# Optimization experiments

Hardware: AMD Instinct MI355X
Metric: run time of the kernel (lower is better)

The kernel has to match this reference:

```python
import jax, jax.numpy as jnp
import numpy as np

B, S, D = 1, 2048, 2048      # batch, seq, hidden_dim
DF = 768                      # moe intermediate (per routed expert)
DSH = 2048                    # shared-expert intermediate
E, K = 32, 8                  # num routed experts, top_k
BLK = 128                     # fp8 block-scale size
CAP = 1024
T = B * S


def _dequant(w, s, blk=BLK):
    # w: [E, M, N] fp8 values (stored fp32), s: [E, M/blk, N/blk] block scales
    Eh, M, N = w.shape
    Mb, Nb = s.shape[1], s.shape[2]
    return (w.reshape(Eh, Mb, blk, Nb, blk) * s[:, :, None, :, None]).reshape(Eh, M, N)


def setup_inputs() -> dict:
    key = jax.random.key(0)
    ks = jax.random.split(key, 13)
    n = lambda k, shp, sc=0.02: jax.random.normal(k, shp, jnp.float32) * sc
    u = lambda k, shp: jax.random.uniform(k, shp, jnp.float32, 0.005, 0.02)
    return {
        "hidden_states": jax.random.normal(ks[0], (B, S, D), jnp.float32),
        "router_w": n(ks[1], (E, D)),
        # raw fp8-value weights (simulated as fp32 integers-in-range values) + block scale_inv
        "wg_fp8": jax.random.normal(ks[2], (E, DF, D), jnp.float32),
        "sg": u(ks[3], (E, DF // BLK, D // BLK)),
        "wu_fp8": jax.random.normal(ks[4], (E, DF, D), jnp.float32),
        "su": u(ks[5], (E, DF // BLK, D // BLK)),
        "wd_fp8": jax.random.normal(ks[6], (E, D, DF), jnp.float32),
        "sd": u(ks[7], (E, D // BLK, DF // BLK)),
        "ws_gate": n(ks[8], (DSH, D)),
        "ws_up": n(ks[9], (DSH, D)),
        "ws_down": n(ks[10], (D, DSH)),
        "w_shared_gate": n(ks[11], (1, D)),
    }


def reference(hidden_states, router_w, wg_fp8, sg, wu_fp8, su, wd_fp8, sd,
              ws_gate, ws_up, ws_down, w_shared_gate):
    x = hidden_states.reshape(-1, D)  # [T, D]

    # shared expert (SwiGLU) + its sigmoid gate
    shared = (jax.nn.silu(x @ ws_gate.T) * (x @ ws_up.T)) @ ws_down.T
    sh_gate = jax.nn.sigmoid(x @ w_shared_gate.T)  # [T, 1]

    # router: softmax -> top-k -> renormalize (Qwen MoE gate)
    probs = jax.nn.softmax(x @ router_w.T, axis=-1)          # [T, E]
    rw, sel = jax.lax.top_k(probs, K)                        # [T, K]
    rw = rw / jnp.sum(rw, axis=-1, keepdims=True)

    # capacity-based dispatch (replaces the python per-expert loop; same math)
    flat_e = sel.reshape(-1)                                 # [T*K]
    oh = jax.nn.one_hot(flat_e, E, dtype=jnp.int32)
    pos = jnp.sum(jnp.cumsum(oh, axis=0) * oh, axis=-1) - 1  # position within expert
    keep = (pos < CAP)
    pos_c = jnp.minimum(pos, CAP)                            # overflow -> scratch slot CAP
    tok = jnp.arange(T * K) // K                             # owning token of each (t,k) pair

    buf = jnp.zeros((E, CAP + 1, D), x.dtype).at[flat_e, pos_c].set(x[tok])

    # block-scale dequant (fp8*scale_inv), then per-expert SwiGLU
    Wg = _dequant(wg_fp8, sg)
    Wu = _dequant(wu_fp8, su)
    Wd = _dequant(wd_fp8, sd)
    g = jnp.einsum('ecd,efd->ecf', buf, Wg)
    up = jnp.einsum('ecd,efd->ecf', buf, Wu)
    h = jax.nn.silu(g) * up
    y = jnp.einsum('ecf,edf->ecd', h, Wd)                    # [E, CAP+1, D]

    # weighted scatter-add back to tokens (index_add_ equivalent)
    y_tok = y[flat_e, pos_c]                                 # [T*K, D]
    w_tok = rw.reshape(-1) * keep.astype(x.dtype)
    out = jax.ops.segment_sum(y_tok * w_tok[:, None], tok, num_segments=T)

    out = out + sh_gate * shared
    return out.reshape(B, S, D)
```

## Files before the change

### kernel.cpp

```cpp
#include <hip/hip_runtime.h>
#include <hip/hip_bf16.h>


#define TT   2048
#define DD   2048
#define DFF  768
#define DSH  2048
#define EE   32
#define KTOP 8
#define CAP  1024

typedef _Float16 half8  __attribute__((ext_vector_type(8)));
typedef _Float16 half4v __attribute__((ext_vector_type(4)));
typedef float    f32x4  __attribute__((ext_vector_type(4)));

__global__ __launch_bounds__(256) void k_init(int* __restrict__ cnt,
                                              int* __restrict__ slot_tok) {
  int i = blockIdx.x * 256 + threadIdx.x;
  if (i < EE * CAP) slot_tok[i] = 0;
  if (i < EE) cnt[i] = 0;
}

__global__ __launch_bounds__(256) void k_cast(const float* __restrict__ in,
                                              _Float16* __restrict__ out) {
  int i = blockIdx.x * 256 + threadIdx.x;
  float4 v = ((const float4*)in)[i];
  half4v h = { (_Float16)v.x, (_Float16)v.y, (_Float16)v.z, (_Float16)v.w };
  ((half4v*)out)[i] = h;
}

__global__ __launch_bounds__(64) void k_router(
    const float* __restrict__ x, const float* __restrict__ rw,
    const float* __restrict__ wshg,
    float* __restrict__ shg, int* __restrict__ cnt,
    int* __restrict__ slot_tok, float* __restrict__ slot_w,
    int* __restrict__ slot_pair, int* __restrict__ pair_pos) {
  int t = blockIdx.x;
  int lane = threadIdx.x;
  const float* xr = x + (size_t)t * DD;
  float xv[32];
#pragma unroll
  for (int j = 0; j < 32; ++j) xv[j] = xr[lane + j * 64];

  __shared__ float lg[EE];
  for (int e = 0; e < EE; ++e) {
    const float* we = rw + (size_t)e * DD;
    float s = 0.f;
#pragma unroll
    for (int j = 0; j < 32; ++j) s += xv[j] * we[lane + j * 64];
#pragma unroll
    for (int off = 32; off > 0; off >>= 1) s += __shfl_down(s, off);
    if (lane == 0) lg[e] = s;
  }
  {
    float s = 0.f;
#pragma unroll
    for (int j = 0; j < 32; ++j) s += xv[j] * wshg[lane + j * 64];
#pragma unroll
    for (int off = 32; off > 0; off >>= 1) s += __shfl_down(s, off);
    if (lane == 0) shg[t] = 1.f / (1.f + expf(-s));
  }
  if (lane == 0) {
    unsigned used = 0;
    int sel[KTOP];
    float val[KTOP];
    for (int k = 0; k < KTOP; ++k) {
      float bv = -1e30f; int bi = 0;
      for (int e = 0; e < EE; ++e)
        if (!((used >> e) & 1) && lg[e] > bv) { bv = lg[e]; bi = e; }
      used |= (1u << bi);
      sel[k] = bi; val[k] = bv;
    }
    float mx = val[0], sum = 0.f;
    for (int k = 0; k < KTOP; ++k) { val[k] = expf(val[k] - mx); sum += val[k]; }
    float inv = 1.f / sum;
    for (int k = 0; k < KTOP; ++k) {
      int e = sel[k];
      int pos = atomicAdd(&cnt[e], 1);
      pair_pos[t * KTOP + k] = pos;
      if (pos < CAP) {
        slot_tok[e * CAP + pos] = t;
        slot_w[e * CAP + pos] = val[k] * inv;
        slot_pair[e * CAP + pos] = t * KTOP + k;
      }
    }
  }
}

template<bool DUAL, bool GATHER, int EPI, int NPB, int MBB, int KDIM>
__global__ __launch_bounds__(256, 2) void k_gemm(
    const _Float16* __restrict__ A,
    const float* __restrict__ B0f, const float* __restrict__ B1f,
    const float* __restrict__ S0, const float* __restrict__ S1,
    int sCols, int sStrideE,
    _Float16* __restrict__ OutH,
    int ldA, int ldOut,
    long long strideAE, long long strideBE, long long strideOE,
    const int* __restrict__ cnt,
    const int* __restrict__ slot_tok, const float* __restrict__ slot_w) {
  constexpr int BK = 64;
  constexpr int KT = KDIM / BK;
  constexpr int NF = DUAL ? 2 : 4;
  constexpr int BN = DUAL ? 64 : 128;
  constexpr int BCH = DUAL ? 4 : 8;

  const int f = blockIdx.x;
  const int xcd = f & 7;
  const int t0 = f >> 3;
  const int mb = t0 % MBB;
  const int pp = t0 / MBB;
  const int p  = pp * 8 + xcd;
  const int nb = p % NPB;
  const int e  = p / NPB;

  int rows = cnt[e] > CAP ? CAP : cnt[e];
  const int rowBase = mb * 128;
  if (rowBase >= rows) return;
  const int nBase = nb * BN;

  const int tid = threadIdx.x;
  const int lane = tid & 63;
  const int wave = tid >> 6;
  const int wr = wave >> 1;
  const int wc = wave & 1;

  __shared__ __align__(16) _Float16 sA[3][8192];
  __shared__ __align__(16) _Float16 sB[2][8192];

  const _Float16* Ae = A + (GATHER ? 0 : (long long)e * strideAE);
  const float* B0e = B0f + (long long)e * strideBE;
  const float* B1e = DUAL ? (B1f + (long long)e * strideBE) : nullptr;
  const float* S0e = S0 + (long long)e * sStrideE;
  const float* S1e = DUAL ? (S1 + (long long)e * sStrideE) : nullptr;
  const int sRow = (nBase >> 7) * sCols;

  int aByte[4];
#pragma unroll
  for (int i = 0; i < 4; ++i) {
    int c = tid + i * 256;
    int row = c >> 3;
    int colB = ((c & 7) << 4) ^ ((row & 7) << 4);
    int src = GATHER ? slot_tok[e * CAP + rowBase + row] : (rowBase + row);
    aByte[i] = src * (2 * ldA) + colB;
  }
  int bOff[BCH], wByte[BCH];
#pragma unroll
  for (int i = 0; i < BCH; ++i) {
    int c = tid + i * 256;
    int rn = c >> 4;
    int c4 = (c & 15) << 2;
    bOff[i] = (nBase + rn) * KDIM + c4;
    wByte[i] = ((rn << 7) + (c4 << 1)) ^ ((rn & 7) << 4);
  }

  f32x4 accG[4][NF];
  f32x4 accU[DUAL ? 4 : 1][NF];
#pragma unroll
  for (int m = 0; m < 4; ++m)
#pragma unroll
    for (int n = 0; n < NF; ++n) {
      accG[m][n] = (f32x4){0.f, 0.f, 0.f, 0.f};
      if constexpr (DUAL) accU[m][n] = (f32x4){0.f, 0.f, 0.f, 0.f};
    }

  auto stageA = [&](int kt, int buf) {
#pragma unroll
    for (int i = 0; i < 4; ++i) {
      __builtin_amdgcn_global_load_lds(
          (const __attribute__((address_space(1))) void*)
              ((const char*)Ae + aByte[i] + kt * (BK * 2)),
          (__attribute__((address_space(3))) void*)&sA[buf][(tid + i * 256) * 8],
          16, 0, 0);
    }
  };
  auto loadB = [&](int kt, float4 (&r0)[BCH], float4 (&r1)[BCH]) {
    const int ko = kt * BK;
#pragma unroll
    for (int i = 0; i < BCH; ++i) r0[i] = *(const float4*)(B0e + bOff[i] + ko);
    if constexpr (DUAL) {
#pragma unroll
      for (int i = 0; i < BCH; ++i) r1[i] = *(const float4*)(B1e + bOff[i] + ko);
    }
  };
  auto storeB = [&](int kt, float4 (&r0)[BCH], float4 (&r1)[BCH]) {
    float s0 = S0e[sRow + (kt >> 1)];
    float s1 = DUAL ? S1e[sRow + (kt >> 1)] : 0.f;
    char* base = (char*)&sB[kt & 1][0];
#pragma unroll
    for (int i = 0; i < BCH; ++i) {
      half4v h = { (_Float16)(r0[i].x * s0), (_Float16)(r0[i].y * s0),
                   (_Float16)(r0[i].z * s0), (_Float16)(r0[i].w * s0) };
      *(half4v*)(base + wByte[i]) = h;
      if constexpr (DUAL) {
        half4v h1 = { (_Float16)(r1[i].x * s1), (_Float16)(r1[i].y * s1),
                      (_Float16)(r1[i].z * s1), (_Float16)(r1[i].w * s1) };
        *(half4v*)(base + 8192 + wByte[i]) = h1;
      }
    }
  };
  auto computeTile = [&](int ia, int ib) {
    const char* pA = (const char*)&sA[ia][0];
    const char* pB = (const char*)&sB[ib][0];
#pragma unroll
    for (int kk = 0; kk < 2; ++kk) {
      const int koff = kk * 32 + (lane >> 4) * 8;
      half8 a[4];
#pragma unroll
      for (int m = 0; m < 4; ++m) {
        int r = wr * 64 + m * 16 + (lane & 15);
        int byt = ((r << 7) + (koff << 1)) ^ ((r & 7) << 4);
        a[m] = *(const half8*)(pA + byt);
      }
      if constexpr (DUAL) {
        half8 bg[2], bu[2];
#pragma unroll
        for (int n = 0; n < 2; ++n) {
          int rn = wc * 32 + n * 16 + (lane & 15);
          int byt = ((rn << 7) + (koff << 1)) ^ ((rn & 7) << 4);
          bg[n] = *(const half8*)(pB + byt);
          bu[n] = *(const half8*)(pB + 8192 + byt);
        }
#pragma unroll
        for (int m = 0; m < 4; ++m)
#pragma unroll
          for (int n = 0; n < 2; ++n) {
            accG[m][n] = __builtin_amdgcn_mfma_f32_16x16x32_f16(a[m], bg[n], accG[m][n], 0, 0, 0);
            accU[m][n] = __builtin_amdgcn_mfma_f32_16x16x32_f16(a[m], bu[n], accU[m][n], 0, 0, 0);
          }
      } else {
        half8 b[4];
#pragma unroll
        for (int n = 0; n < 4; ++n) {
          int rn = wc * 64 + n * 16 + (lane & 15);
          int byt = ((rn << 7) + (koff << 1)) ^ ((rn & 7) << 4);
          b[n] = *(const half8*)(pB + byt);
        }
#pragma unroll
        for (int m = 0; m < 4; ++m)
#pragma unroll
          for (int n = 0; n < 4; ++n)
            accG[m][n] = __builtin_amdgcn_mfma_f32_16x16x32_f16(a[m], b[n], accG[m][n], 0, 0, 0);
      }
    }
  };

  float4 rbE0[BCH], rbE1[BCH], rbO0[BCH], rbO1[BCH];

  loadB(0, rbE0, rbE1);
  loadB(1, rbO0, rbO1);
  stageA(0, 0);
  stageA(1, 1);
  __builtin_amdgcn_sched_barrier(0);
  storeB(0, rbE0, rbE1);
  asm volatile("s_waitcnt lgkmcnt(0)" ::: "memory");
  asm volatile("s_waitcnt vmcnt(4)" ::: "memory");
  __builtin_amdgcn_s_barrier();
  __builtin_amdgcn_sched_barrier(0);

  int bufC = 0, bufW = 2;
  for (int kt = 0; kt < KT; ++kt) {
    if (kt + 2 < KT) {
      stageA(kt + 2, bufW);
      if (kt & 1) loadB(kt + 2, rbO0, rbO1);
      else        loadB(kt + 2, rbE0, rbE1);
      __builtin_amdgcn_sched_barrier(0);
    }
    computeTile(bufC, kt & 1);
    if (kt + 1 < KT) {
      if (kt & 1) storeB(kt + 1, rbE0, rbE1);
      else        storeB(kt + 1, rbO0, rbO1);
    }
    asm volatile("s_waitcnt lgkmcnt(0)" ::: "memory");
    if (kt + 2 < KT) { asm volatile("s_waitcnt vmcnt(12)" ::: "memory"); }
    else             { asm volatile("s_waitcnt vmcnt(0)"  ::: "memory"); }
    __builtin_amdgcn_s_barrier();
    __builtin_amdgcn_sched_barrier(0);
    bufC = (bufC == 2) ? 0 : bufC + 1;
    bufW = (bufW == 2) ? 0 : bufW + 1;
  }

#pragma unroll
  for (int m = 0; m < 4; ++m) {
#pragma unroll
    for (int i = 0; i < 4; ++i) {
      int row = rowBase + wr * 64 + m * 16 + (lane >> 4) * 4 + i;
      if (row < rows) {
        if constexpr (EPI == 1) {
          int pair = slot_tok[e * CAP + row];
          float w = slot_w[e * CAP + row];
#pragma unroll
          for (int n = 0; n < NF; ++n) {
            int col = nBase + wc * 64 + n * 16 + (lane & 15);
            OutH[(long long)pair * DD + col] = (_Float16)(w * accG[m][n][i]);
          }
        } else {
          long long outBase = (long long)e * strideOE;
#pragma unroll
          for (int n = 0; n < NF; ++n) {
            int col = nBase + (DUAL ? wc * 32 : wc * 64) + n * 16 + (lane & 15);
            long long o = outBase + (long long)row * ldOut + col;
            if constexpr (DUAL) {
              float gv = accG[m][n][i];
              float uv = accU[m][n][i];
              OutH[o] = (_Float16)((gv / (1.f + __expf(-gv))) * uv);
            } else {
              OutH[o] = (_Float16)accG[m][n][i];
            }
          }
        }
      }
    }
  }
}

template<bool DUAL, int EPI, int NPB, int MBB, int KDIM>
__global__ __launch_bounds__(256, 2) void k_gemm16(
    const _Float16* __restrict__ A,
    const _Float16* __restrict__ B0h, const _Float16* __restrict__ B1h,
    _Float16* __restrict__ OutH, float* __restrict__ OutF,
    const float* __restrict__ shg,
    int ldA, int ldOut, int rowsConst) {
  constexpr int BK = 64;
  constexpr int KT = KDIM / BK;
  constexpr int NF = DUAL ? 2 : 4;
  constexpr int BN = DUAL ? 64 : 128;

  const int f = blockIdx.x;
  const int xcd = f & 7;
  const int t0 = f >> 3;
  const int mb = t0 % MBB;
  const int pp = t0 / MBB;
  const int p  = pp * 8 + xcd;
  const int nb = p % NPB;

  int rows = rowsConst;
  const int rowBase = mb * 128;
  if (rowBase >= rows) return;
  const int nBase = nb * BN;

  const int tid = threadIdx.x;
  const int lane = tid & 63;
  const int wave = tid >> 6;
  const int wr = wave >> 1;
  const int wc = wave & 1;

  __shared__ __align__(16) _Float16 sA[3][8192];
  __shared__ __align__(16) _Float16 sB[2][8192];

  int aByte[4];
#pragma unroll
  for (int i = 0; i < 4; ++i) {
    int c = tid + i * 256;
    int row = c >> 3;
    int colB = ((c & 7) << 4) ^ ((row & 7) << 4);
    aByte[i] = (rowBase + row) * (2 * ldA) + colB;
  }
  int bByte[4];
#pragma unroll
  for (int i = 0; i < 4; ++i) {
    int c = tid + i * 256;
    int rn = DUAL ? ((c & 511) >> 3) : (c >> 3);
    int colB = ((c & 7) << 4) ^ ((rn & 7) << 4);
    bByte[i] = (nBase + rn) * (2 * KDIM) + colB;
  }

  f32x4 accG[4][NF];
  f32x4 accU[DUAL ? 4 : 1][NF];
#pragma unroll
  for (int m = 0; m < 4; ++m)
#pragma unroll
    for (int n = 0; n < NF; ++n) {
      accG[m][n] = (f32x4){0.f, 0.f, 0.f, 0.f};
      if constexpr (DUAL) accU[m][n] = (f32x4){0.f, 0.f, 0.f, 0.f};
    }

  auto stageA = [&](int kt, int buf) {
#pragma unroll
    for (int i = 0; i < 4; ++i) {
      __builtin_amdgcn_global_load_lds(
          (const __attribute__((address_space(1))) void*)
              ((const char*)A + aByte[i] + kt * 128),
          (__attribute__((address_space(3))) void*)&sA[buf][(tid + i * 256) * 8],
          16, 0, 0);
    }
  };
  auto stageB = [&](int kt, int buf) {
#pragma unroll
    for (int i = 0; i < 4; ++i) {
      const _Float16* src = (DUAL && i >= 2) ? B1h : B0h;
      __builtin_amdgcn_global_load_lds(
          (const __attribute__((address_space(1))) void*)
              ((const char*)src + bByte[i] + kt * 128),
          (__attribute__((address_space(3))) void*)&sB[buf][(tid + i * 256) * 8],
          16, 0, 0);
    }
  };
  auto computeTile = [&](int ia, int ib) {
    const char* pA = (const char*)&sA[ia][0];
    const char* pB = (const char*)&sB[ib][0];
#pragma unroll
    for (int kk = 0; kk < 2; ++kk) {
      const int koff = kk * 32 + (lane >> 4) * 8;
      half8 a[4];
#pragma unroll
      for (int m = 0; m < 4; ++m) {
        int r = wr * 64 + m * 16 + (lane & 15);
        int byt = ((r << 7) + (koff << 1)) ^ ((r & 7) << 4);
        a[m] = *(const half8*)(pA + byt);
      }
      if constexpr (DUAL) {
        half8 bg[2], bu[2];
#pragma unroll
        for (int n = 0; n < 2; ++n) {
          int rn = wc * 32 + n * 16 + (lane & 15);
          int byt = ((rn << 7) + (koff << 1)) ^ ((rn & 7) << 4);
          bg[n] = *(const half8*)(pB + byt);
          bu[n] = *(const half8*)(pB + 8192 + byt);
        }
#pragma unroll
        for (int m = 0; m < 4; ++m)
#pragma unroll
          for (int n = 0; n < 2; ++n) {
            accG[m][n] = __builtin_amdgcn_mfma_f32_16x16x32_f16(a[m], bg[n], accG[m][n], 0, 0, 0);
            accU[m][n] = __builtin_amdgcn_mfma_f32_16x16x32_f16(a[m], bu[n], accU[m][n], 0, 0, 0);
          }
      } else {
        half8 b[4];
#pragma unroll
        for (int n = 0; n < 4; ++n) {
          int rn = wc * 64 + n * 16 + (lane & 15);
          int byt = ((rn << 7) + (koff << 1)) ^ ((rn & 7) << 4);
          b[n] = *(const half8*)(pB + byt);
        }
#pragma unroll
        for (int m = 0; m < 4; ++m)
#pragma unroll
          for (int n = 0; n < 4; ++n)
            accG[m][n] = __builtin_amdgcn_mfma_f32_16x16x32_f16(a[m], b[n], accG[m][n], 0, 0, 0);
      }
    }
  };

  stageB(0, 0);
  __builtin_amdgcn_sched_barrier(0);
  stageA(0, 0);
  __builtin_amdgcn_sched_barrier(0);
  stageA(1, 1);
  __builtin_amdgcn_sched_barrier(0);

  int bufC = 0, bufW = 2;
  for (int kt = 0; kt < KT; ++kt) {
    asm volatile("s_waitcnt lgkmcnt(0)" ::: "memory");
    if (kt + 1 < KT) { asm volatile("s_waitcnt vmcnt(4)" ::: "memory"); }
    else             { asm volatile("s_waitcnt vmcnt(0)" ::: "memory"); }
    __builtin_amdgcn_sched_barrier(0);
    __builtin_amdgcn_s_barrier();
    __builtin_amdgcn_sched_barrier(0);
    if (kt + 1 < KT) stageB(kt + 1, (kt + 1) & 1);
    if (kt + 2 < KT) stageA(kt + 2, bufW);
    __builtin_amdgcn_sched_barrier(0);
    computeTile(bufC, kt & 1);
    bufC = (bufC == 2) ? 0 : bufC + 1;
    bufW = (bufW == 2) ? 0 : bufW + 1;
  }

#pragma unroll
  for (int m = 0; m < 4; ++m) {
#pragma unroll
    for (int i = 0; i < 4; ++i) {
      int row = rowBase + wr * 64 + m * 16 + (lane >> 4) * 4 + i;
      if (row < rows) {
        if constexpr (EPI == 2) {
          float g = shg[row];
#pragma unroll
          for (int n = 0; n < NF; ++n) {
            int col = nBase + wc * 64 + n * 16 + (lane & 15);
            OutF[(long long)row * DD + col] += g * accG[m][n][i];
          }
        } else {
#pragma unroll
          for (int n = 0; n < NF; ++n) {
            int col = nBase + (DUAL ? wc * 32 : wc * 64) + n * 16 + (lane & 15);
            long long o = (long long)row * ldOut + col;
            if constexpr (DUAL) {
              float gv = accG[m][n][i];
              float uv = accU[m][n][i];
              OutH[o] = (_Float16)((gv / (1.f + __expf(-gv))) * uv);
            } else {
              OutH[o] = (_Float16)accG[m][n][i];
            }
          }
        }
      }
    }
  }
}

__global__ __launch_bounds__(256) void k_combine(
    const _Float16* __restrict__ Yp, const int* __restrict__ pair_pos,
    float* __restrict__ out) {
  int t = blockIdx.x;
  int col = threadIdx.x * 8;
  float acc[8] = {0.f, 0.f, 0.f, 0.f, 0.f, 0.f, 0.f, 0.f};
#pragma unroll
  for (int k = 0; k < KTOP; ++k) {
    if (pair_pos[t * KTOP + k] < CAP) {
      half8 y = *(const half8*)&Yp[((size_t)t * KTOP + k) * DD + col];
#pragma unroll
      for (int j = 0; j < 8; ++j) acc[j] += (float)y[j];
    }
  }
  float4 o0 = {acc[0], acc[1], acc[2], acc[3]};
  float4 o1 = {acc[4], acc[5], acc[6], acc[7]};
  *(float4*)&out[(size_t)t * DD + col] = o0;
  *(float4*)&out[(size_t)t * DD + col + 4] = o1;
}

extern "C" void kernel_launch(void* const* d_in, const int* in_sizes, int n_in,
                              void* d_out, int out_size, void* d_ws, size_t ws_size,
                              hipStream_t stream) {
  (void)in_sizes; (void)n_in; (void)out_size; (void)ws_size;
  const float* x    = (const float*)d_in[0];
  const float* rw   = (const float*)d_in[1];
  const float* wg   = (const float*)d_in[2];
  const float* sg   = (const float*)d_in[3];
  const float* wu   = (const float*)d_in[4];
  const float* su   = (const float*)d_in[5];
  const float* wd   = (const float*)d_in[6];
  const float* sd   = (const float*)d_in[7];
  const float* wsg  = (const float*)d_in[8];
  const float* wsu  = (const float*)d_in[9];
  const float* wsd  = (const float*)d_in[10];
  const float* wshg = (const float*)d_in[11];
  float* out = (float*)d_out;

  char* p = (char*)d_ws;
  auto alloc = [&](size_t bytes) {
    char* r = p;
    p += (bytes + 255) & ~(size_t)255;
    return r;
  };
  _Float16* x_h   = (_Float16*)alloc((size_t)TT * DD * 2);
  _Float16* H     = (_Float16*)alloc((size_t)EE * CAP * DFF * 2);
  _Float16* Hsh   = (_Float16*)alloc((size_t)TT * DSH * 2);
  _Float16* Yp    = (_Float16*)alloc((size_t)TT * KTOP * DD * 2);
  _Float16* wsg_h = (_Float16*)alloc((size_t)DSH * DD * 2);
  _Float16* wsu_h = (_Float16*)alloc((size_t)DSH * DD * 2);
  _Float16* wsd_h = (_Float16*)alloc((size_t)DD * DSH * 2);
  float* shg      = (float*)alloc((size_t)TT * 4);
  int* cnt        = (int*)alloc((size_t)EE * 4);
  int* slot_tok   = (int*)alloc((size_t)EE * CAP * 4);
  float* slot_w   = (float*)alloc((size_t)EE * CAP * 4);
  int* slot_pair  = (int*)alloc((size_t)EE * CAP * 4);
  int* pair_pos   = (int*)alloc((size_t)TT * KTOP * 4);

  k_init<<<(EE * CAP + 255) / 256, 256, 0, stream>>>(cnt, slot_tok);
  k_cast<<<(TT * DD / 4) / 256, 256, 0, stream>>>(x, x_h);
  k_cast<<<(DSH * DD / 4) / 256, 256, 0, stream>>>(wsg, wsg_h);
  k_cast<<<(DSH * DD / 4) / 256, 256, 0, stream>>>(wsu, wsu_h);
  k_cast<<<(DD * DSH / 4) / 256, 256, 0, stream>>>(wsd, wsd_h);
  k_router<<<TT, 64, 0, stream>>>(x, rw, wshg, shg, cnt, slot_tok, slot_w,
                                  slot_pair, pair_pos);

  k_gemm<true, true, 0, 12, 8, DD><<<3072, 256, 0, stream>>>(
      x_h, wg, wu, sg, su, DD / 128, (DFF / 128) * (DD / 128),
      H, DD, DFF,
      0LL, (long long)DFF * DD, (long long)CAP * DFF,
      cnt, slot_tok, nullptr);

  k_gemm<false, false, 1, 16, 8, DFF><<<4096, 256, 0, stream>>>(
      H, wd, wd, sd, sd, DFF / 128, (DD / 128) * (DFF / 128),
      Yp, DFF, DD,
      (long long)CAP * DFF, (long long)DD * DFF, 0LL,
      cnt, slot_pair, slot_w);

  k_combine<<<TT, 256, 0, stream>>>(Yp, pair_pos, out);

  k_gemm16<true, 0, 32, 16, DD><<<512, 256, 0, stream>>>(
      x_h, wsg_h, wsu_h, Hsh, nullptr, nullptr,
      DD, DSH, TT);

  k_gemm16<false, 2, 16, 16, DSH><<<256, 256, 0, stream>>>(
      Hsh, wsd_h, wsd_h, nullptr, out, shg,
      DSH, DD, TT);
}
```

Before: 762.2 us.

## Merge MoE and shared-expert GEMMs into two heterogeneous mega-kernels with predequantized down weights

The routed gate/up GEMM, the shared-expert gate/up GEMM and a dequantization pass that turns the fp32 down-projection weights into fp16 are merged into one launch, with blocks split by block index. A second launch runs the routed down-projection (now reading fp16 weights through direct global-to-LDS loads) alongside the shared down-projection. The shared-expert gating is folded into the combine kernel. The aim is to fill the GPU with concurrent work and cut launch count and the per-tile fp32 dequant in the down GEMM. In exchange it adds an extra pass writing a full fp16 copy of the down weights, and it reuses the shared-gate weight buffer as scratch output.

```diff
diff --git a/kernel.cpp b/kernel.cpp
--- a/kernel.cpp
+++ b/kernel.cpp
@@ -87,131 +87,117 @@
   }
 }
 
-template<bool DUAL, bool GATHER, int EPI, int NPB, int MBB, int KDIM>
-__global__ __launch_bounds__(256, 2) void k_gemm(
-    const _Float16* __restrict__ A,
-    const float* __restrict__ B0f, const float* __restrict__ B1f,
-    const float* __restrict__ S0, const float* __restrict__ S1,
-    int sCols, int sStrideE,
-    _Float16* __restrict__ OutH,
-    int ldA, int ldOut,
-    long long strideAE, long long strideBE, long long strideOE,
-    const int* __restrict__ cnt,
-    const int* __restrict__ slot_tok, const float* __restrict__ slot_w) {
-  constexpr int BK = 64;
-  constexpr int KT = KDIM / BK;
-  constexpr int NF = DUAL ? 2 : 4;
-  constexpr int BN = DUAL ? 64 : 128;
-  constexpr int BCH = DUAL ? 4 : 8;
-
-  const int f = blockIdx.x;
-  const int xcd = f & 7;
-  const int t0 = f >> 3;
-  const int mb = t0 % MBB;
-  const int pp = t0 / MBB;
-  const int p  = pp * 8 + xcd;
-  const int nb = p % NPB;
-  const int e  = p / NPB;
-
-  int rows = cnt[e] > CAP ? CAP : cnt[e];
-  const int rowBase = mb * 128;
-  if (rowBase >= rows) return;
-  const int nBase = nb * BN;
+__global__ __launch_bounds__(256, 2) void k_megaA(
+    const _Float16* __restrict__ x_h,
+    const float* __restrict__ wg, const float* __restrict__ wu,
+    const float* __restrict__ sg, const float* __restrict__ su,
+    _Float16* __restrict__ H,
+    const int* __restrict__ cnt, const int* __restrict__ slot_tok,
+    const _Float16* __restrict__ wsg_h, const _Float16* __restrict__ wsu_h,
+    _Float16* __restrict__ Hsh,
+    const float* __restrict__ wd, const float* __restrict__ sd,
+    _Float16* __restrict__ wd_h) {
+  __shared__ __align__(16) _Float16 sA[3][8192];
+  __shared__ __align__(16) _Float16 sB[2][8192];
 
   const int tid = threadIdx.x;
+  const int bid = blockIdx.x;
+
+  if (bid >= 3584) {
+    const long long tot4 = (long long)EE * DD * DFF / 4;
+    long long idx = (long long)(bid - 3584) * 256 + tid;
+    for (; idx < tot4; idx += 512LL * 256) {
+      long long b = idx * 4;
+      int e = (int)(b / ((long long)DD * DFF));
+      int rem = (int)(b - (long long)e * DD * DFF);
+      int r = rem / DFF;
+      int c = rem - r * DFF;
+      float sc = sd[e * ((DD / 128) * (DFF / 128)) + (r >> 7) * (DFF / 128) + (c >> 7)];
+      float4 v = ((const float4*)wd)[idx];
+      half4v h = { (_Float16)(v.x * sc), (_Float16)(v.y * sc),
+                   (_Float16)(v.z * sc), (_Float16)(v.w * sc) };
+      ((half4v*)wd_h)[idx] = h;
+    }
+    return;
+  }
+
   const int lane = tid & 63;
   const int wave = tid >> 6;
   const int wr = wave >> 1;
   const int wc = wave & 1;
 
-  __shared__ __align__(16) _Float16 sA[3][8192];
-  __shared__ __align__(16) _Float16 sB[2][8192];
-
-  const _Float16* Ae = A + (GATHER ? 0 : (long long)e * strideAE);
-  const float* B0e = B0f + (long long)e * strideBE;
-  const float* B1e = DUAL ? (B1f + (long long)e * strideBE) : nullptr;
-  const float* S0e = S0 + (long long)e * sStrideE;
-  const float* S1e = DUAL ? (S1 + (long long)e * sStrideE) : nullptr;
-  const int sRow = (nBase >> 7) * sCols;
-
-  int aByte[4];
-#pragma unroll
-  for (int i = 0; i < 4; ++i) {
-    int c = tid + i * 256;
-    int row = c >> 3;
-    int colB = ((c & 7) << 4) ^ ((row & 7) << 4);
-    int src = GATHER ? slot_tok[e * CAP + rowBase + row] : (rowBase + row);
-    aByte[i] = src * (2 * ldA) + colB;
-  }
-  int bOff[BCH], wByte[BCH];
-#pragma unroll
-  for (int i = 0; i < BCH; ++i) {
-    int c = tid + i * 256;
-    int rn = c >> 4;
-    int c4 = (c & 15) << 2;
-    bOff[i] = (nBase + rn) * KDIM + c4;
-    wByte[i] = ((rn << 7) + (c4 << 1)) ^ ((rn & 7) << 4);
-  }
-
-  f32x4 accG[4][NF];
-  f32x4 accU[DUAL ? 4 : 1][NF];
-#pragma unroll
-  for (int m = 0; m < 4; ++m)
-#pragma unroll
-    for (int n = 0; n < NF; ++n) {
-      accG[m][n] = (f32x4){0.f, 0.f, 0.f, 0.f};
-      if constexpr (DUAL) accU[m][n] = (f32x4){0.f, 0.f, 0.f, 0.f};
-    }
-
-  auto stageA = [&](int kt, int buf) {
+  if (bid >= 3072) {
+    constexpr int KT = DD / 64;
+    const int f = bid - 3072;
+    const int xcd = f & 7;
+    const int t0 = f >> 3;
+    const int mb = t0 % 16;
+    const int pp = t0 / 16;
+    const int p  = pp * 8 + xcd;
+    const int nb = p % 32;
+    const int rowBase = mb * 128;
+    const int nBase = nb * 64;
+
+    int aByte[4];
 #pragma unroll
     for (int i = 0; i < 4; ++i) {
-      __builtin_amdgcn_global_load_lds(
-          (const __attribute__((address_space(1))) void*)
-              ((const char*)Ae + aByte[i] + kt * (BK * 2)),
-          (__attribute__((address_space(3))) void*)&sA[buf][(tid + i * 256) * 8],
-          16, 0, 0);
-    }
-  };
-  auto loadB = [&](int kt, float4 (&r0)[BCH], float4 (&r1)[BCH]) {
-    const int ko = kt * BK;
-#pragma unroll
-    for (int i = 0; i < BCH; ++i) r0[i] = *(const float4*)(B0e + bOff[i] + ko);
-    if constexpr (DUAL) {
-#pragma unroll
-      for (int i = 0; i < BCH; ++i) r1[i] = *(const float4*)(B1e + bOff[i] + ko);
-    }
-  };
-  auto storeB = [&](int kt, float4 (&r0)[BCH], float4 (&r1)[BCH]) {
-    float s0 = S0e[sRow + (kt >> 1)];
-    float s1 = DUAL ? S1e[sRow + (kt >> 1)] : 0.f;
-    char* base = (char*)&sB[kt & 1][0];
-#pragma unroll
-    for (int i = 0; i < BCH; ++i) {
-      half4v h = { (_Float16)(r0[i].x * s0), (_Float16)(r0[i].y * s0),
-                   (_Float16)(r0[i].z * s0), (_Float16)(r0[i].w * s0) };
-      *(half4v*)(base + wByte[i]) = h;
-      if constexpr (DUAL) {
-        half4v h1 = { (_Float16)(r1[i].x * s1), (_Float16)(r1[i].y * s1),
-                      (_Float16)(r1[i].z * s1), (_Float16)(r1[i].w * s1) };
-        *(half4v*)(base + 8192 + wByte[i]) = h1;
-      }
-    }
-  };
-  auto computeTile = [&](int ia, int ib) {
-    const char* pA = (const char*)&sA[ia][0];
-    const char* pB = (const char*)&sB[ib][0];
-#pragma unroll
-    for (int kk = 0; kk < 2; ++kk) {
-      const int koff = kk * 32 + (lane >> 4) * 8;
-      half8 a[4];
-#pragma unroll
-      for (int m = 0; m < 4; ++m) {
-        int r = wr * 64 + m * 16 + (lane & 15);
-        int byt = ((r << 7) + (koff << 1)) ^ ((r & 7) << 4);
-        a[m] = *(const half8*)(pA + byt);
-      }
-      if constexpr (DUAL) {
+      int c = tid + i * 256;
+      int row = c >> 3;
+      int colB = ((c & 7) << 4) ^ ((row & 7) << 4);
+      aByte[i] = (rowBase + row) * (2 * DD) + colB;
+    }
+    int bByte[4];
+#pragma unroll
+    for (int i = 0; i < 4; ++i) {
+      int c = tid + i * 256;
+      int rn = (c & 511) >> 3;
+      int colB = ((c & 7) << 4) ^ ((rn & 7) << 4);
+      bByte[i] = (nBase + rn) * (2 * DD) + colB;
+    }
+
+    f32x4 accG[4][2], accU[4][2];
+#pragma unroll
+    for (int m = 0; m < 4; ++m)
+#pragma unroll
+      for (int n = 0; n < 2; ++n) {
+        accG[m][n] = (f32x4){0.f, 0.f, 0.f, 0.f};
+        accU[m][n] = (f32x4){0.f, 0.f, 0.f, 0.f};
+      }
+
+    auto stageA = [&](int kt, int buf) {
+#pragma unroll
+      for (int i = 0; i < 4; ++i) {
+        __builtin_amdgcn_global_load_lds(
+            (const __attribute__((address_space(1))) void*)
+                ((const char*)x_h + aByte[i] + kt * 128),
+            (__attribute__((address_space(3))) void*)&sA[buf][(tid + i * 256) * 8],
+            16, 0, 0);
+      }
+    };
+    auto stageB = [&](int kt, int buf) {
+#pragma unroll
+      for (int i = 0; i < 4; ++i) {
+        const _Float16* src = (i >= 2) ? wsu_h : wsg_h;
+        __builtin_amdgcn_global_load_lds(
+            (const __attribute__((address_space(1))) void*)
+                ((const char*)src + bByte[i] + kt * 128),
+            (__attribute__((address_space(3))) void*)&sB[buf][(tid + i * 256) * 8],
+            16, 0, 0);
+      }
+    };
+    auto computeTile = [&](int ia, int ib) {
+      const char* pA = (const char*)&sA[ia][0];
+      const char* pB = (const char*)&sB[ib][0];
+#pragma unroll
+      for (int kk = 0; kk < 2; ++kk) {
+        const int koff = kk * 32 + (lane >> 4) * 8;
+        half8 a[4];
+#pragma unroll
+        for (int m = 0; m < 4; ++m) {
+          int r = wr * 64 + m * 16 + (lane & 15);
+          int byt = ((r << 7) + (koff << 1)) ^ ((r & 7) << 4);
+          a[m] = *(const half8*)(pA + byt);
+        }
         half8 bg[2], bu[2];
 #pragma unroll
         for (int n = 0; n < 2; ++n) {
@@ -227,188 +213,144 @@
             accG[m][n] = __builtin_amdgcn_mfma_f32_16x16x32_f16(a[m], bg[n], accG[m][n], 0, 0, 0);
             accU[m][n] = __builtin_amdgcn_mfma_f32_16x16x32_f16(a[m], bu[n], accU[m][n], 0, 0, 0);
           }
-      } else {
-        half8 b[4];
-#pragma unroll
-        for (int n = 0; n < 4; ++n) {
-          int rn = wc * 64 + n * 16 + (lane & 15);
-          int byt = ((rn << 7) + (koff << 1)) ^ ((rn & 7) << 4);
-          b[n] = *(const half8*)(pB + byt);
+      }
+    };
+
+    stageB(0, 0);
+    __builtin_amdgcn_sched_barrier(0);
+    stageA(0, 0);
+    __builtin_amdgcn_sched_barrier(0);
+    stageA(1, 1);
+    __builtin_amdgcn_sched_barrier(0);
+
+    int bufC = 0, bufW = 2;
+    for (int kt = 0; kt < KT; ++kt) {
+      asm volatile("s_waitcnt lgkmcnt(0)" ::: "memory");
+      if (kt + 1 < KT) { asm volatile("s_waitcnt vmcnt(4)" ::: "memory"); }
+      else             { asm volatile("s_waitcnt vmcnt(0)" ::: "memory"); }
+      __builtin_amdgcn_sched_barrier(0);
+      __builtin_amdgcn_s_barrier();
+      __builtin_amdgcn_sched_barrier(0);
+      if (kt + 1 < KT) stageB(kt + 1, (kt + 1) & 1);
+      if (kt + 2 < KT) stageA(kt + 2, bufW);
+      __builtin_amdgcn_sched_barrier(0);
+      computeTile(bufC, kt & 1);
+      bufC = (bufC == 2) ? 0 : bufC + 1;
+      bufW = (bufW == 2) ? 0 : bufW + 1;
+    }
+
+#pragma unroll
+    for (int m = 0; m < 4; ++m)
+#pragma unroll
+      for (int i = 0; i < 4; ++i) {
+        int row = rowBase + wr * 64 + m * 16 + (lane >> 4) * 4 + i;
+#pragma unroll
+        for (int n = 0; n < 2; ++n) {
+          int col = nBase + wc * 32 + n * 16 + (lane & 15);
+          float gv = accG[m][n][i];
+          float uv = accU[m][n][i];
+          Hsh[(long long)row * DSH + col] =
+              (_Float16)((gv / (1.f + __expf(-gv))) * uv);
         }
-#pragma unroll
-        for (int m = 0; m < 4; ++m)
-#pragma unroll
-          for (int n = 0; n < 4; ++n)
-            accG[m][n] = __builtin_amdgcn_mfma_f32_16x16x32_f16(a[m], b[n], accG[m][n], 0, 0, 0);
-      }
-    }
-  };
-
-  float4 rbE0[BCH], rbE1[BCH], rbO0[BCH], rbO1[BCH];
-
-  loadB(0, rbE0, rbE1);
-  loadB(1, rbO0, rbO1);
-  stageA(0, 0);
-  stageA(1, 1);
-  __builtin_amdgcn_sched_barrier(0);
-  storeB(0, rbE0, rbE1);
-  asm volatile("s_waitcnt lgkmcnt(0)" ::: "memory");
-  asm volatile("s_waitcnt vmcnt(4)" ::: "memory");
-  __builtin_amdgcn_s_barrier();
-  __builtin_amdgcn_sched_barrier(0);
-
-  int bufC = 0, bufW = 2;
-  for (int kt = 0; kt < KT; ++kt) {
-    if (kt + 2 < KT) {
-      stageA(kt + 2, bufW);
-      if (kt & 1) loadB(kt + 2, rbO0, rbO1);
-      else        loadB(kt + 2, rbE0, rbE1);
-      __builtin_amdgcn_sched_barrier(0);
-    }
-    computeTile(bufC, kt & 1);
-    if (kt + 1 < KT) {
-      if (kt & 1) storeB(kt + 1, rbE0, rbE1);
-      else        storeB(kt + 1, rbO0, rbO1);
-    }
-    asm volatile("s_waitcnt lgkmcnt(0)" ::: "memory");
-    if (kt + 2 < KT) { asm volatile("s_waitcnt vmcnt(12)" ::: "memory"); }
-    else             { asm volatile("s_waitcnt vmcnt(0)"  ::: "memory"); }
-    __builtin_amdgcn_s_barrier();
-    __builtin_amdgcn_sched_barrier(0);
-    bufC = (bufC == 2) ? 0 : bufC + 1;
-    bufW = (bufW == 2) ? 0 : bufW + 1;
-  }
-
-#pragma unroll
-  for (int m = 0; m < 4; ++m) {
+      }
+    return;
+  }
+
+  {
+    constexpr int KT = DD / 64;
+    constexpr int BCH = 4;
+    const int f = bid;
+    const int xcd = f & 7;
+    const int t0 = f >> 3;
+    const int mb = t0 % 8;
+    const int pp = t0 / 8;
+    const int p  = pp * 8 + xcd;
+    const int nb = p % 12;
+    const int e  = p / 12;
+
+    int rows = cnt[e] > CAP ? CAP : cnt[e];
+    const int rowBase = mb * 128;
+    if (rowBase >= rows) return;
+    const int nBase = nb * 64;
+
+    const float* B0e = wg + (long long)e * DFF * DD;
+    const float* B1e = wu + (long long)e * DFF * DD;
+    const float* S0e = sg + (long long)e * ((DFF / 128) * (DD / 128));
+    const float* S1e = su + (long long)e * ((DFF / 128) * (DD / 128));
+    const int sRow = (nBase >> 7) * (DD / 128);
+
+    int aByte[4];
 #pragma unroll
     for (int i = 0; i < 4; ++i) {
-      int row = rowBase + wr * 64 + m * 16 + (lane >> 4) * 4 + i;
-      if (row < rows) {
-        if constexpr (EPI == 1) {
-          int pair = slot_tok[e * CAP + row];
-          float w = slot_w[e * CAP + row];
-#pragma unroll
-          for (int n = 0; n < NF; ++n) {
-            int col = nBase + wc * 64 + n * 16 + (lane & 15);
-            OutH[(long long)pair * DD + col] = (_Float16)(w * accG[m][n][i]);
-          }
-        } else {
-          long long outBase = (long long)e * strideOE;
-#pragma unroll
-          for (int n = 0; n < NF; ++n) {
-            int col = nBase + (DUAL ? wc * 32 : wc * 64) + n * 16 + (lane & 15);
-            long long o = outBase + (long long)row * ldOut + col;
-            if constexpr (DUAL) {
-              float gv = accG[m][n][i];
-              float uv = accU[m][n][i];
-              OutH[o] = (_Float16)((gv / (1.f + __expf(-gv))) * uv);
-            } else {
-              OutH[o] = (_Float16)accG[m][n][i];
-            }
-          }
+      int c = tid + i * 256;
+      int row = c >> 3;
+      int colB = ((c & 7) << 4) ^ ((row & 7) << 4);
+      int src = slot_tok[e * CAP + rowBase + row];
+      aByte[i] = src * (2 * DD) + colB;
+    }
+    int bOff[BCH], wByte[BCH];
+#pragma unroll
+    for (int i = 0; i < BCH; ++i) {
+      int c = tid + i * 256;
+      int rn = c >> 4;
+      int c4 = (c & 15) << 2;
+      bOff[i] = (nBase + rn) * DD + c4;
+      wByte[i] = ((rn << 7) + (c4 << 1)) ^ ((rn & 7) << 4);
+    }
+
+    f32x4 accG[4][2], accU[4][2];
+#pragma unroll
+    for (int m = 0; m < 4; ++m)
+#pragma unroll
+      for (int n = 0; n < 2; ++n) {
+        accG[m][n] = (f32x4){0.f, 0.f, 0.f, 0.f};
+        accU[m][n] = (f32x4){0.f, 0.f, 0.f, 0.f};
+      }
+
+    auto stageA = [&](int kt, int buf) {
+#pragma unroll
+      for (int i = 0; i < 4; ++i) {
+        __builtin_amdgcn_global_load_lds(
+            (const __attribute__((address_space(1))) void*)
+                ((const char*)x_h + aByte[i] + kt * 128),
+            (__attribute__((address_space(3))) void*)&sA[buf][(tid + i * 256) * 8],
+            16, 0, 0);
+      }
+    };
+    auto loadB = [&](int kt, float4 (&r0)[BCH], float4 (&r1)[BCH]) {
+      const int ko = kt * 64;
+#pragma unroll
+      for (int i = 0; i < BCH; ++i) r0[i] = *(const float4*)(B0e + bOff[i] + ko);
+#pragma unroll
+      for (int i = 0; i < BCH; ++i) r1[i] = *(const float4*)(B1e + bOff[i] + ko);
+    };
+    auto storeB = [&](int kt, float4 (&r0)[BCH], float4 (&r1)[BCH]) {
+      float s0 = S0e[sRow + (kt >> 1)];
+      float s1 = S1e[sRow + (kt >> 1)];
+      char* base = (char*)&sB[kt & 1][0];
+#pragma unroll
+      for (int i = 0; i < BCH; ++i) {
+        half4v h = { (_Float16)(r0[i].x * s0), (_Float16)(r0[i].y * s0),
+                     (_Float16)(r0[i].z * s0), (_Float16)(r0[i].w * s0) };
+        *(half4v*)(base + wByte[i]) = h;
+        half4v h1 = { (_Float16)(r1[i].x * s1), (_Float16)(r1[i].y * s1),
+                      (_Float16)(r1[i].z * s1), (_Float16)(r1[i].w * s1) };
+        *(half4v*)(base + 8192 + wByte[i]) = h1;
+      }
+    };
+    auto computeTile = [&](int ia, int ib) {
+      const char* pA = (const char*)&sA[ia][0];
+      const char* pB = (const char*)&sB[ib][0];
+#pragma unroll
+      for (int kk = 0; kk < 2; ++kk) {
+        const int koff = kk * 32 + (lane >> 4) * 8;
+        half8 a[4];
+#pragma unroll
+        for (int m = 0; m < 4; ++m) {
+          int r = wr * 64 + m * 16 + (lane & 15);
+          int byt = ((r << 7) + (koff << 1)) ^ ((r & 7) << 4);
+          a[m] = *(const half8*)(pA + byt);
         }
-      }
-    }
-  }
-}
-
-template<bool DUAL, int EPI, int NPB, int MBB, int KDIM>
-__global__ __launch_bounds__(256, 2) void k_gemm16(
-    const _Float16* __restrict__ A,
-    const _Float16* __restrict__ B0h, const _Float16* __restrict__ B1h,
-    _Float16* __restrict__ OutH, float* __restrict__ OutF,
-    const float* __restrict__ shg,
-    int ldA, int ldOut, int rowsConst) {
-  constexpr int BK = 64;
-  constexpr int KT = KDIM / BK;
-  constexpr int NF = DUAL ? 2 : 4;
-  constexpr int BN = DUAL ? 64 : 128;
-
-  const int f = blockIdx.x;
-  const int xcd = f & 7;
-  const int t0 = f >> 3;
-  const int mb = t0 % MBB;
-  const int pp = t0 / MBB;
-  const int p  = pp * 8 + xcd;
-  const int nb = p % NPB;
-
-  int rows = rowsConst;
-  const int rowBase = mb * 128;
-  if (rowBase >= rows) return;
-  const int nBase = nb * BN;
-
-  const int tid = threadIdx.x;
-  const int lane = tid & 63;
-  const int wave = tid >> 6;
-  const int wr = wave >> 1;
-  const int wc = wave & 1;
-
-  __shared__ __align__(16) _Float16 sA[3][8192];
-  __shared__ __align__(16) _Float16 sB[2][8192];
-
-  int aByte[4];
-#pragma unroll
-  for (int i = 0; i < 4; ++i) {
-    int c = tid + i * 256;
-    int row = c >> 3;
-    int colB = ((c & 7) << 4) ^ ((row & 7) << 4);
-    aByte[i] = (rowBase + row) * (2 * ldA) + colB;
-  }
-  int bByte[4];
-#pragma unroll
-  for (int i = 0; i < 4; ++i) {
-    int c = tid + i * 256;
-    int rn = DUAL ? ((c & 511) >> 3) : (c >> 3);
-    int colB = ((c & 7) << 4) ^ ((rn & 7) << 4);
-    bByte[i] = (nBase + rn) * (2 * KDIM) + colB;
-  }
-
-  f32x4 accG[4][NF];
-  f32x4 accU[DUAL ? 4 : 1][NF];
-#pragma unroll
-  for (int m = 0; m < 4; ++m)
-#pragma unroll
-    for (int n = 0; n < NF; ++n) {
-      accG[m][n] = (f32x4){0.f, 0.f, 0.f, 0.f};
-      if constexpr (DUAL) accU[m][n] = (f32x4){0.f, 0.f, 0.f, 0.f};
-    }
-
-  auto stageA = [&](int kt, int buf) {
-#pragma unroll
-    for (int i = 0; i < 4; ++i) {
-      __builtin_amdgcn_global_load_lds(
-          (const __attribute__((address_space(1))) void*)
-              ((const char*)A + aByte[i] + kt * 128),
-          (__attribute__((address_space(3))) void*)&sA[buf][(tid + i * 256) * 8],
-          16, 0, 0);
-    }
-  };
-  auto stageB = [&](int kt, int buf) {
-#pragma unroll
-    for (int i = 0; i < 4; ++i) {
-      const _Float16* src = (DUAL && i >= 2) ? B1h : B0h;
-      __builtin_amdgcn_global_load_lds(
-          (const __attribute__((address_space(1))) void*)
-              ((const char*)src + bByte[i] + kt * 128),
-          (__attribute__((address_space(3))) void*)&sB[buf][(tid + i * 256) * 8],
-          16, 0, 0);
-    }
-  };
-  auto computeTile = [&](int ia, int ib) {
-    const char* pA = (const char*)&sA[ia][0];
-    const char* pB = (const char*)&sB[ib][0];
-#pragma unroll
-    for (int kk = 0; kk < 2; ++kk) {
-      const int koff = kk * 32 + (lane >> 4) * 8;
-      half8 a[4];
-#pragma unroll
-      for (int m = 0; m < 4; ++m) {
-        int r = wr * 64 + m * 16 + (lane & 15);
-        int byt = ((r << 7) + (koff << 1)) ^ ((r & 7) << 4);
-        a[m] = *(const half8*)(pA + byt);
-      }
-      if constexpr (DUAL) {
         half8 bg[2], bu[2];
 #pragma unroll
         for (int n = 0; n < 2; ++n) {
@@ -424,20 +366,186 @@
             accG[m][n] = __builtin_amdgcn_mfma_f32_16x16x32_f16(a[m], bg[n], accG[m][n], 0, 0, 0);
             accU[m][n] = __builtin_amdgcn_mfma_f32_16x16x32_f16(a[m], bu[n], accU[m][n], 0, 0, 0);
           }
-      } else {
-        half8 b[4];
-#pragma unroll
-        for (int n = 0; n < 4; ++n) {
-          int rn = wc * 64 + n * 16 + (lane & 15);
-          int byt = ((rn << 7) + (koff << 1)) ^ ((rn & 7) << 4);
-          b[n] = *(const half8*)(pB + byt);
+      }
+    };
+
+    float4 rbE0[BCH], rbE1[BCH], rbO0[BCH], rbO1[BCH];
+
+    stageA(0, 0); loadB(0, rbE0, rbE1);
+    __builtin_amdgcn_sched_barrier(0);
+    stageA(1, 1); loadB(1, rbO0, rbO1);
+    __builtin_amdgcn_sched_barrier(0);
+
+    int bufC = 0, bufW = 2;
+    for (int kt = 0; kt < KT; kt += 2) {
+      if (kt + 1 < KT) { asm volatile("s_waitcnt vmcnt(12)" ::: "memory"); }
+      else             { asm volatile("s_waitcnt vmcnt(0)"  ::: "memory"); }
+      __builtin_amdgcn_sched_barrier(0);
+      storeB(kt, rbE0, rbE1);
+      asm volatile("s_waitcnt lgkmcnt(0)" ::: "memory");
+      __builtin_amdgcn_sched_barrier(0);
+      __builtin_amdgcn_s_barrier();
+      __builtin_amdgcn_sched_barrier(0);
+      if (kt + 2 < KT) { stageA(kt + 2, bufW); loadB(kt + 2, rbE0, rbE1); }
+      __builtin_amdgcn_sched_barrier(0);
+      computeTile(bufC, 0);
+      bufC = (bufC == 2) ? 0 : bufC + 1;
+      bufW = (bufW == 2) ? 0 : bufW + 1;
+
+      if (kt + 2 < KT) { asm volatile("s_waitcnt vmcnt(12)" ::: "memory"); }
+      else             { asm volatile("s_waitcnt vmcnt(0)"  ::: "memory"); }
+      __builtin_amdgcn_sched_barrier(0);
+      storeB(kt + 1, rbO0, rbO1);
+      asm volatile("s_waitcnt lgkmcnt(0)" ::: "memory");
+      __builtin_amdgcn_sched_barrier(0);
+      __builtin_amdgcn_s_barrier();
+      __builtin_amdgcn_sched_barrier(0);
+      if (kt + 3 < KT) { stageA(kt + 3, bufW); loadB(kt + 3, rbO0, rbO1); }
+      __builtin_amdgcn_sched_barrier(0);
+      computeTile(bufC, 1);
+      bufC = (bufC == 2) ? 0 : bufC + 1;
+      bufW = (bufW == 2) ? 0 : bufW + 1;
+    }
+
+#pragma unroll
+    for (int m = 0; m < 4; ++m)
+#pragma unroll
+      for (int i = 0; i < 4; ++i) {
+        int row = rowBase + wr * 64 + m * 16 + (lane >> 4) * 4 + i;
+        if (row < rows) {
+#pragma unroll
+          for (int n = 0; n < 2; ++n) {
+            int col = nBase + wc * 32 + n * 16 + (lane & 15);
+            float gv = accG[m][n][i];
+            float uv = accU[m][n][i];
+            H[(long long)e * CAP * DFF + (long long)row * DFF + col] =
+                (_Float16)((gv / (1.f + __expf(-gv))) * uv);
+          }
         }
-#pragma unroll
-        for (int m = 0; m < 4; ++m)
-#pragma unroll
-          for (int n = 0; n < 4; ++n)
-            accG[m][n] = __builtin_amdgcn_mfma_f32_16x16x32_f16(a[m], b[n], accG[m][n], 0, 0, 0);
-      }
+      }
+  }
+}
+
+__global__ __launch_bounds__(256, 2) void k_megaB(
+    const _Float16* __restrict__ H, const _Float16* __restrict__ wd_h,
+    _Float16* __restrict__ Yp,
+    const int* __restrict__ cnt,
+    const int* __restrict__ slot_pair, const float* __restrict__ slot_w,
+    const _Float16* __restrict__ Hsh, const _Float16* __restrict__ wsd_h,
+    _Float16* __restrict__ Ysh) {
+  __shared__ __align__(16) _Float16 sA[3][8192];
+  __shared__ __align__(16) _Float16 sB[2][8192];
+
+  const int tid = threadIdx.x;
+  const int bid = blockIdx.x;
+  const int lane = tid & 63;
+  const int wave = tid >> 6;
+  const int wr = wave >> 1;
+  const int wc = wave & 1;
+
+  const _Float16 *Ab, *Bb;
+  _Float16* Outp;
+  int KDIM, KT, rows, ldA, e = 0, nb, mb;
+  bool scatter;
+  if (bid < 4096) {
+    int xcd = bid & 7, t0 = bid >> 3;
+    mb = t0 % 8;
+    int pp = t0 / 8;
+    int p = pp * 8 + xcd;
+    nb = p % 16;
+    e = p / 16;
+    rows = cnt[e] > CAP ? CAP : cnt[e];
+    scatter = true;
+    Ab = H + (long long)e * CAP * DFF;
+    Bb = wd_h + (long long)e * DD * DFF;
+    KDIM = DFF; KT = DFF / 64; ldA = DFF;
+    Outp = Yp;
+  } else {
+    int f2 = bid - 4096;
+    int xcd = f2 & 7, t0 = f2 >> 3;
+    mb = t0 % 16;
+    int pp = t0 / 16;
+    int p = pp * 8 + xcd;
+    nb = p % 16;
+    rows = TT;
+    scatter = false;
+    Ab = Hsh;
+    Bb = wsd_h;
+    KDIM = DSH; KT = DSH / 64; ldA = DSH;
+    Outp = Ysh;
+  }
+  const int rowBase = mb * 128;
+  if (rowBase >= rows) return;
+  const int nBase = nb * 128;
+
+  int aByte[4];
+#pragma unroll
+  for (int i = 0; i < 4; ++i) {
+    int c = tid + i * 256;
+    int row = c >> 3;
+    int colB = ((c & 7) << 4) ^ ((row & 7) << 4);
+    aByte[i] = (rowBase + row) * (2 * ldA) + colB;
+  }
+  int bByte[4];
+#pragma unroll
+  for (int i = 0; i < 4; ++i) {
+    int c = tid + i * 256;
+    int rn = c >> 3;
+    int colB = ((c & 7) << 4) ^ ((rn & 7) << 4);
+    bByte[i] = (nBase + rn) * (2 * KDIM) + colB;
+  }
+
+  f32x4 acc[4][4];
+#pragma unroll
+  for (int m = 0; m < 4; ++m)
+#pragma unroll
+    for (int n = 0; n < 4; ++n) acc[m][n] = (f32x4){0.f, 0.f, 0.f, 0.f};
+
+  auto stageA = [&](int kt, int buf) {
+#pragma unroll
+    for (int i = 0; i < 4; ++i) {
+      __builtin_amdgcn_global_load_lds(
+          (const __attribute__((address_space(1))) void*)
+              ((const char*)Ab + aByte[i] + kt * 128),
+          (__attribute__((address_space(3))) void*)&sA[buf][(tid + i * 256) * 8],
+          16, 0, 0);
+    }
+  };
+  auto stageB = [&](int kt, int buf) {
+#pragma unroll
+    for (int i = 0; i < 4; ++i) {
+      __builtin_amdgcn_global_load_lds(
+          (const __attribute__((address_space(1))) void*)
+              ((const char*)Bb + bByte[i] + kt * 128),
+          (__attribute__((address_space(3))) void*)&sB[buf][(tid + i * 256) * 8],
+          16, 0, 0);
+    }
+  };
+  auto computeTile = [&](int ia, int ib) {
+    const char* pA = (const char*)&sA[ia][0];
+    const char* pB = (const char*)&sB[ib][0];
+#pragma unroll
+    for (int kk = 0; kk < 2; ++kk) {
+      const int koff = kk * 32 + (lane >> 4) * 8;
+      half8 a[4];
+#pragma unroll
+      for (int m = 0; m < 4; ++m) {
+        int r = wr * 64 + m * 16 + (lane & 15);
+        int byt = ((r << 7) + (koff << 1)) ^ ((r & 7) << 4);
+        a[m] = *(const half8*)(pA + byt);
+      }
+      half8 b[4];
+#pragma unroll
+      for (int n = 0; n < 4; ++n) {
+        int rn = wc * 64 + n * 16 + (lane & 15);
+        int byt = ((rn << 7) + (koff << 1)) ^ ((rn & 7) << 4);
+        b[n] = *(const half8*)(pB + byt);
+      }
+#pragma unroll
+      for (int m = 0; m < 4; ++m)
+#pragma unroll
+        for (int n = 0; n < 4; ++n)
+          acc[m][n] = __builtin_amdgcn_mfma_f32_16x16x32_f16(a[m], b[n], acc[m][n], 0, 0, 0);
     }
   };
 
@@ -465,43 +573,41 @@
   }
 
 #pragma unroll
-  for (int m = 0; m < 4; ++m) {
+  for (int m = 0; m < 4; ++m)
 #pragma unroll
     for (int i = 0; i < 4; ++i) {
       int row = rowBase + wr * 64 + m * 16 + (lane >> 4) * 4 + i;
       if (row < rows) {
-        if constexpr (EPI == 2) {
-          float g = shg[row];
-#pragma unroll
-          for (int n = 0; n < NF; ++n) {
+        if (scatter) {
+          int pair = slot_pair[e * CAP + row];
+          float w = slot_w[e * CAP + row];
+#pragma unroll
+          for (int n = 0; n < 4; ++n) {
             int col = nBase + wc * 64 + n * 16 + (lane & 15);
-            OutF[(long long)row * DD + col] += g * accG[m][n][i];
+            Outp[(long long)pair * DD + col] = (_Float16)(w * acc[m][n][i]);
           }
         } else {
 #pragma unroll
-          for (int n = 0; n < NF; ++n) {
-            int col = nBase + (DUAL ? wc * 32 : wc * 64) + n * 16 + (lane & 15);
-            long long o = (long long)row * ldOut + col;
-            if constexpr (DUAL) {
-              float gv = accG[m][n][i];
-              float uv = accU[m][n][i];
-              OutH[o] = (_Float16)((gv / (1.f + __expf(-gv))) * uv);
-            } else {
-              OutH[o] = (_Float16)accG[m][n][i];
-            }
+          for (int n = 0; n < 4; ++n) {
+            int col = nBase + wc * 64 + n * 16 + (lane & 15);
+            Outp[(long long)row * DD + col] = (_Float16)acc[m][n][i];
           }
         }
       }
     }
-  }
 }
 
-__global__ __launch_bounds__(256) void k_combine(
-    const _Float16* __restrict__ Yp, const int* __restrict__ pair_pos,
+__global__ __launch_bounds__(256) void k_combine2(
+    const _Float16* __restrict__ Yp, const _Float16* __restrict__ Ysh,
+    const float* __restrict__ shg, const int* __restrict__ pair_pos,
     float* __restrict__ out) {
   int t = blockIdx.x;
   int col = threadIdx.x * 8;
-  float acc[8] = {0.f, 0.f, 0.f, 0.f, 0.f, 0.f, 0.f, 0.f};
+  float acc[8];
+  half8 ys = *(const half8*)&Ysh[(size_t)t * DD + col];
+  float g = shg[t];
+#pragma unroll
+  for (int j = 0; j < 8; ++j) acc[j] = g * (float)ys[j];
 #pragma unroll
   for (int k = 0; k < KTOP; ++k) {
     if (pair_pos[t * KTOP + k] < CAP) {
@@ -544,6 +650,7 @@
   _Float16* H     = (_Float16*)alloc((size_t)EE * CAP * DFF * 2);
   _Float16* Hsh   = (_Float16*)alloc((size_t)TT * DSH * 2);
   _Float16* Yp    = (_Float16*)alloc((size_t)TT * KTOP * DD * 2);
+  _Float16* wd_h  = (_Float16*)alloc((size_t)EE * DD * DFF * 2);
   _Float16* wsg_h = (_Float16*)alloc((size_t)DSH * DD * 2);
   _Float16* wsu_h = (_Float16*)alloc((size_t)DSH * DD * 2);
   _Float16* wsd_h = (_Float16*)alloc((size_t)DD * DSH * 2);
@@ -554,6 +661,8 @@
   int* slot_pair  = (int*)alloc((size_t)EE * CAP * 4);
   int* pair_pos   = (int*)alloc((size_t)TT * KTOP * 4);
 
+  _Float16* Ysh = wsg_h;
+
   k_init<<<(EE * CAP + 255) / 256, 256, 0, stream>>>(cnt, slot_tok);
   k_cast<<<(TT * DD / 4) / 256, 256, 0, stream>>>(x, x_h);
   k_cast<<<(DSH * DD / 4) / 256, 256, 0, stream>>>(wsg, wsg_h);
@@ -562,25 +671,11 @@
   k_router<<<TT, 64, 0, stream>>>(x, rw, wshg, shg, cnt, slot_tok, slot_w,
                                   slot_pair, pair_pos);
 
-  k_gemm<true, true, 0, 12, 8, DD><<<3072, 256, 0, stream>>>(
-      x_h, wg, wu, sg, su, DD / 128, (DFF / 128) * (DD / 128),
-      H, DD, DFF,
-      0LL, (long long)DFF * DD, (long long)CAP * DFF,
-      cnt, slot_tok, nullptr);
-
-  k_gemm<false, false, 1, 16, 8, DFF><<<4096, 256, 0, stream>>>(
-      H, wd, wd, sd, sd, DFF / 128, (DD / 128) * (DFF / 128),
-      Yp, DFF, DD,
-      (long long)CAP * DFF, (long long)DD * DFF, 0LL,
-      cnt, slot_pair, slot_w);
-
-  k_combine<<<TT, 256, 0, stream>>>(Yp, pair_pos, out);
-
-  k_gemm16<true, 0, 32, 16, DD><<<512, 256, 0, stream>>>(
-      x_h, wsg_h, wsu_h, Hsh, nullptr, nullptr,
-      DD, DSH, TT);
-
-  k_gemm16<false, 2, 16, 16, DSH><<<256, 256, 0, stream>>>(
-      Hsh, wsd_h, wsd_h, nullptr, out, shg,
-      DSH, DD, TT);
+  k_megaA<<<4096, 256, 0, stream>>>(x_h, wg, wu, sg, su, H, cnt, slot_tok,
+                                    wsg_h, wsu_h, Hsh, wd, sd, wd_h);
+
+  k_megaB<<<4352, 256, 0, stream>>>(H, wd_h, Yp, cnt, slot_pair, slot_w,
+                                    Hsh, wsd_h, Ysh);
+
+  k_combine2<<<TT, 256, 0, stream>>>(Yp, Ysh, shg, pair_pos, out);
 }
```

Result: faster. 704.4 us (-7.6%).
